# Optimization experiments

Measured on AMD Instinct MI355X. Metric: run time of the kernel, lower is better.

The kernel has to match this reference:

```python
import jax, jax.numpy as jnp
import numpy as np

B = 16; V = 30522; D = 512; H = 8; DH = 64; FF = 2048
NC = 4; NF = 30; NN = 34; FL = 64; HL = 32; NLAYERS = 2

def _pos_encoding(L, d):
    pos = np.arange(L)[:, None].astype(np.float32)
    i = np.arange(0, d, 2)[None, :].astype(np.float32)
    ang = pos / np.power(10000.0, i / d)
    pe = np.zeros((L, d), dtype=np.float32)
    pe[:, 0::2] = np.sin(ang)
    pe[:, 1::2] = np.cos(ang)
    return jnp.asarray(pe)

def _ln(x, g, b):
    m = x.mean(-1, keepdims=True)
    v = ((x - m) ** 2).mean(-1, keepdims=True)
    return (x - m) / jnp.sqrt(v + 1e-5) * g + b

def _encoder(ids, emb, Wqkv, bqkv, Wo, bo, ln1_g, ln1_b, Wff1, bff1, Wff2, bff2, ln2_g, ln2_b):
    Bx, L = ids.shape
    x = emb[ids] * jnp.sqrt(jnp.float32(D)) + _pos_encoding(L, D)
    for l in range(NLAYERS):  # torch post-norm encoder layer, relu FFN
        qkv = x @ Wqkv[l] + bqkv[l]
        q, k, v = jnp.split(qkv, 3, axis=-1)
        q = q.reshape(Bx, L, H, DH); k = k.reshape(Bx, L, H, DH); v = v.reshape(Bx, L, H, DH)
        att = jax.nn.softmax(jnp.einsum('blhd,bmhd->bhlm', q, k) / jnp.sqrt(jnp.float32(DH)), axis=-1)
        o = jnp.einsum('bhlm,bmhd->blhd', att, v).reshape(Bx, L, D) @ Wo[l] + bo[l]
        x = _ln(x + o, ln1_g[l], ln1_b[l])
        f = jax.nn.relu(x @ Wff1[l] + bff1[l]) @ Wff2[l] + bff2[l]
        x = _ln(x + f, ln2_g[l], ln2_b[l])
    return x

def _masked_mean(emb, mask):
    m = mask[..., None]
    return (emb * m).sum(1) / jnp.clip(m.sum(1), 1e-9, None)

def _solve_edges(W, adj, iters=100, lr=0.05, c=10.0):
    # differentiable proxy for the CvxpyLayer SDP relaxation: projected gradient
    # ascent on symmetric E in [0,1], maximizing sum(W*E) with quadratic penalties
    # for sum(adj*E) <= 6 and trace(E[:4,:4]) == 1 (PSD constraint dropped).
    diag4 = jnp.zeros((NN, NN)).at[jnp.arange(NC), jnp.arange(NC)].set(1.0)
    E0 = jnp.full(W.shape, 0.5)
    def step(E, _):
        s = jnp.sum(adj * E, axis=(1, 2), keepdims=True)
        d = jnp.sum(E * diag4, axis=(1, 2), keepdims=True)
        g = W - 2.0 * c * jax.nn.relu(s - 6.0) * adj - 2.0 * c * (d - 1.0) * diag4
        En = E + lr * g
        En = jnp.clip(0.5 * (En + jnp.swapaxes(En, 1, 2)), 0.0, 1.0)
        return En, None
    E, _ = jax.lax.scan(step, E0, None, length=iters)
    return E

def setup_inputs():
    key = jax.random.key(0)
    ks = jax.random.split(key, 24)
    w = lambda k, shape: (jax.random.normal(k, shape) * 0.02).astype(jnp.float32)
    return {
        'hypothesis_input_ids': jax.random.randint(ks[0], (B, NC, HL), 0, V),
        'hypothesis_attention_mask': jnp.ones((B, NC, HL), jnp.float32),
        'fact_attention_mask': jnp.ones((B, NF, FL), jnp.float32),
        'fact_input_ids': jax.random.randint(ks[1], (B, NF, FL), 0, V),
        'grounding_grounding_overlap': jax.random.uniform(ks[2], (B, NN, NN)),
        'abstract_abstract_overlap': jax.random.uniform(ks[3], (B, NN, NN)),
        'abstract_abstract_similarity': jax.random.uniform(ks[4], (B, NN, NN)),
        'question_grounding_overlap': jax.random.uniform(ks[5], (B, NN, NN)),
        'question_abstract_overlap': jax.random.uniform(ks[6], (B, NN, NN)),
        'question_abstract_similarity': jax.random.uniform(ks[7], (B, NN, NN)),
        'grounding_abstract_overlap': jax.random.uniform(ks[8], (B, NN, NN)),
        'question_question_score': w(ks[9], (B, NN, NN)),
        'labels': jax.random.randint(ks[10], (B,), 0, NC),
        'gold_similarity_scores': jax.random.normal(ks[11], (B, NC, NF)),
        'emb_table': w(ks[12], (V, D)),
        'Wqkv': w(ks[13], (NLAYERS, D, 3 * D)), 'bqkv': jnp.zeros((NLAYERS, 3 * D)),
        'Wo': w(ks[14], (NLAYERS, D, D)), 'bo': jnp.zeros((NLAYERS, D)),
        'ln1_g': jnp.ones((NLAYERS, D)), 'ln1_b': jnp.zeros((NLAYERS, D)),
        'Wff1': w(ks[15], (NLAYERS, D, FF)), 'bff1': jnp.zeros((NLAYERS, FF)),
        'Wff2': w(ks[16], (NLAYERS, FF, D)), 'bff2': jnp.zeros((NLAYERS, D)),
        'ln2_g': jnp.ones((NLAYERS, D)), 'ln2_b': jnp.zeros((NLAYERS, D)),
        'score_W': w(ks[17], (4 * D,)), 'score_b': jnp.zeros(()),
        'abs_score_W': w(ks[18], (4 * D,)), 'abs_score_b': jnp.zeros(()),
        'p_aa_overlap': jnp.ones(()), 'p_aa_sim': jnp.ones(()),
        'p_qa_overlap': jnp.ones(()), 'p_qa_sim': jnp.ones(()),
    }

def reference(hypothesis_input_ids, hypothesis_attention_mask, fact_attention_mask, fact_input_ids,
              grounding_grounding_overlap, abstract_abstract_overlap, abstract_abstract_similarity,
              question_grounding_overlap, question_abstract_overlap, question_abstract_similarity,
              grounding_abstract_overlap, question_question_score, labels, gold_similarity_scores,
              emb_table, Wqkv, bqkv, Wo, bo, ln1_g, ln1_b, Wff1, bff1, Wff2, bff2, ln2_g, ln2_b,
              score_W, score_b, abs_score_W, abs_score_b, p_aa_overlap, p_aa_sim, p_qa_overlap, p_qa_sim):
    enc = lambda ids: _encoder(ids, emb_table, Wqkv, bqkv, Wo, bo, ln1_g, ln1_b,
                               Wff1, bff1, Wff2, bff2, ln2_g, ln2_b)
    fseq = _masked_mean(enc(fact_input_ids.reshape(-1, FL)),
                        fact_attention_mask.reshape(-1, FL)).reshape(-1, NF, D)
    hseq = _masked_mean(enc(hypothesis_input_ids.reshape(-1, HL)),
                        hypothesis_attention_mask.reshape(-1, HL)).reshape(-1, NC, D)
    # abstract-abstract pairwise: concat(f_j, f_i, |f_j-f_i|, f_j*f_i) @ abs_score_W, done chunk-wise
    A1, A2, A3, A4 = jnp.split(abs_score_W, 4)
    aa = (fseq @ A1)[:, None, :] + (fseq @ A2)[:, :, None] \
       + jnp.einsum('bijd,d->bij', jnp.abs(fseq[:, None, :, :] - fseq[:, :, None, :]), A3) \
       + jnp.einsum('bid,bjd->bij', fseq * A4, fseq) + abs_score_b
    aa_sm = jax.nn.softmax(aa.reshape(-1, NF * NF), axis=1).reshape(-1, NF, NF)
    aa_sm = aa_sm * (1.0 - jnp.eye(NF))  # zero diagonal
    aa_sim = abstract_abstract_similarity.at[:, NC:, NC:].set(aa_sm)
    # question-abstract pairwise: concat(f_k, h_c, |f_k-h_c|, f_k*h_c) @ score_W
    S1, S2, S3, S4 = jnp.split(score_W, 4)
    qa = (fseq @ S1)[:, None, :] + (hseq @ S2)[:, :, None] \
       + jnp.einsum('bckd,d->bck', jnp.abs(fseq[:, None, :, :] - hseq[:, :, None, :]), S3) \
       + jnp.einsum('bkd,bcd->bck', fseq * S4, hseq) + score_b
    similarity_scores = jax.nn.softmax(qa, axis=2)  # [B, NC, NF]
    qa_sim = jnp.zeros_like(grounding_abstract_overlap)
    qa_sim = qa_sim.at[:, NC:, :NC].set(jnp.transpose(similarity_scores, (0, 2, 1)))
    qa_sim = qa_sim.at[:, :NC, NC:].set(similarity_scores)
    edge_weights = (-p_aa_overlap * abstract_abstract_overlap + p_aa_sim * aa_sim
                    + p_qa_overlap * question_abstract_overlap + p_qa_sim * qa_sim
                    + question_question_score)
    adj = (edge_weights != 0).astype(jnp.float32)
    edges = _solve_edges(edge_weights, adj)
    final_pred = jnp.diagonal(edges[:, :NC, :NC], axis1=1, axis2=2)  # [B, NC]
    gold = jax.nn.softmax(gold_similarity_scores, axis=2)
    logp = jax.nn.log_softmax(final_pred, axis=1)
    ce = -jnp.mean(logp[jnp.arange(final_pred.shape[0]), labels])
    mse = jnp.mean((similarity_scores - gold) ** 2)
    return ce + mse, final_pred
```

## Files before the change

### kernel.cpp

```cpp
#include <hip/hip_runtime.h>
#include <cstdint>
#include <cstddef>


using u16 = unsigned short;

typedef __bf16 bf16x8 __attribute__((ext_vector_type(8)));
typedef float  floatx4 __attribute__((ext_vector_type(4)));

#if defined(__has_builtin)
#if __has_builtin(__builtin_amdgcn_global_load_lds)
#define USE_GLL 1
#endif
#endif

__device__ __forceinline__ float bf2f(u16 u) {
  return __uint_as_float(((unsigned)u) << 16);
}
__device__ __forceinline__ u16 f2bf(float f) {
  unsigned u = __float_as_uint(f);
  u += 0x7FFFu + ((u >> 16) & 1u);
  return (u16)(u >> 16);
}
__device__ __forceinline__ float ldf(const void* p, size_t i, int isb) {
  return isb ? bf2f(((const u16*)p)[i]) : ((const float*)p)[i];
}

__device__ __forceinline__ float waveSum(float v) {
#pragma unroll
  for (int o = 32; o > 0; o >>= 1) v += __shfl_xor(v, o, 64);
  return v;
}
__device__ __forceinline__ float waveMax(float v) {
#pragma unroll
  for (int o = 32; o > 0; o >>= 1) v = fmaxf(v, __shfl_xor(v, o, 64));
  return v;
}
__device__ __forceinline__ float blockSum(float v, float* sh4) {
  v = waveSum(v);
  if ((threadIdx.x & 63) == 0) sh4[threadIdx.x >> 6] = v;
  __syncthreads();
  float r = sh4[0] + sh4[1] + sh4[2] + sh4[3];
  __syncthreads();
  return r;
}
__device__ __forceinline__ float blockMax(float v, float* sh4) {
  v = waveMax(v);
  if ((threadIdx.x & 63) == 0) sh4[threadIdx.x >> 6] = v;
  __syncthreads();
  float r = fmaxf(fmaxf(sh4[0], sh4[1]), fmaxf(sh4[2], sh4[3]));
  __syncthreads();
  return r;
}

__global__ void detect_kernel(const void* __restrict__ ln1g, int* __restrict__ flag) {
  unsigned u = *(const unsigned*)ln1g;
  *flag = (u == 0x3F800000u) ? 0 : 1;
}

__global__ __launch_bounds__(256) void pe_kernel(float* __restrict__ petab) {
  const int pos = blockIdx.x;
  const float LOG1E4_OVER_D = 9.210340371976184f / 512.0f;
  for (int d = threadIdx.x; d < 512; d += 256) {
    int i2 = d & ~1;
    float ang = (float)pos * expf(-(float)i2 * LOG1E4_OVER_D);
    petab[pos * 512 + d] = (d & 1) ? cosf(ang) : sinf(ang);
  }
}

__global__ __launch_bounds__(256) void transpose_kernel(const void* __restrict__ src,
                                                        u16* __restrict__ dst,
                                                        int K, int N,
                                                        size_t srcz, size_t dstz,
                                                        const int* __restrict__ F) {
  const int isb = *F;
  __shared__ u16 tile[32][33];
  size_t eoff = (size_t)blockIdx.z * srcz;
  u16* d = dst + (size_t)blockIdx.z * dstz;
  int bx = blockIdx.x, by = blockIdx.y;
  int tx = threadIdx.x & 31, ty = threadIdx.x >> 5;
  for (int i = ty; i < 32; i += 8)
    tile[i][tx] = f2bf(ldf(src, eoff + (size_t)(by * 32 + i) * N + bx * 32 + tx, isb));
  __syncthreads();
  for (int i = ty; i < 32; i += 8)
    d[(size_t)(bx * 32 + i) * K + by * 32 + tx] = tile[tx][i];
}

__global__ __launch_bounds__(256) void embed_kernel(const int* __restrict__ ids,
                                                    const void* __restrict__ emb,
                                                    u16* __restrict__ x, int L,
                                                    const float* __restrict__ petab,
                                                    const int* __restrict__ F) {
  const int isb = *F;
  int tok = blockIdx.x;
  int pos = tok % L;
  int id = ids[tok];
  for (int d = threadIdx.x; d < 512; d += 256) {
    float e = ldf(emb, (size_t)id * 512 + d, isb) * 22.62741699796952f;
    x[(size_t)tok * 512 + d] = f2bf(e + petab[pos * 512 + d]);
  }
}

__global__ __launch_bounds__(256) void embed2_kernel(const int* __restrict__ fids,
                                                     const int* __restrict__ hids,
                                                     const void* __restrict__ emb,
                                                     u16* __restrict__ x,
                                                     const float* __restrict__ petab,
                                                     const int* __restrict__ F) {
  const int isb = *F;
  int tok = blockIdx.x;
  int id, pos;
  if (tok < 30720) { id = fids[tok]; pos = tok & 63; }
  else             { int t2 = tok - 30720; id = hids[t2]; pos = t2 & 31; }
  for (int d = threadIdx.x; d < 512; d += 256) {
    float e = ldf(emb, (size_t)id * 512 + d, isb) * 22.62741699796952f;
    x[(size_t)tok * 512 + d] = f2bf(e + petab[pos * 512 + d]);
  }
}

template <int RELU>
__global__ __launch_bounds__(256, 2) void gemm_bt(const u16* __restrict__ A,
                                                  const u16* __restrict__ Bt,
                                                  const void* __restrict__ bias,
                                                  u16* __restrict__ C,
                                                  int M, int N, int K, size_t boff,
                                                  const int* __restrict__ F) {
  const int isb = *F;
  __shared__ __align__(16) u16 As[128 * 64];
  __shared__ __align__(16) u16 Bs[128 * 64];
  const int tid = threadIdx.x;
  const int lane = tid & 63;
  const int wave = tid >> 6;
  const int wm = wave >> 1, wn = wave & 1;
  const int l15 = lane & 15, quad = lane >> 4;

  const int nwg = gridDim.x * gridDim.y;
  const int hw  = blockIdx.y * gridDim.x + blockIdx.x;
  int lg;
  if ((nwg & 7) == 0) {
    lg = (hw & 7) * (nwg >> 3) + (hw >> 3);
  } else {
    int q = nwg >> 3, r = nwg & 7;
    int xcd = hw & 7, j = hw >> 3;
    lg = (xcd < r ? xcd * (q + 1) : r * (q + 1) + (xcd - r) * q) + j;
  }
  const int bm = lg / gridDim.x;
  const int bn = lg - bm * gridDim.x;

  floatx4 acc[4][4];
#pragma unroll
  for (int i = 0; i < 4; i++)
#pragma unroll
    for (int j = 0; j < 4; j++) acc[i][j] = (floatx4){0.f, 0.f, 0.f, 0.f};

  const u16* Abase = A + (size_t)bm * 128 * K;
  const u16* Bbase = Bt + (size_t)bn * 128 * K;

  for (int kt = 0; kt < K; kt += 64) {
#pragma unroll
    for (int i = 0; i < 4; i++) {
      int c = i * 256 + tid;
      int row = c >> 3, p = c & 7;
      int col = (((p - row) & 7)) * 8;
      const u16* ga = &Abase[(size_t)row * K + kt + col];
      const u16* gb = &Bbase[(size_t)row * K + kt + col];
#ifdef USE_GLL
      __builtin_amdgcn_global_load_lds(
          (const __attribute__((address_space(1))) void*)ga,
          (__attribute__((address_space(3))) void*)&As[c * 8], 16, 0, 0);
      __builtin_amdgcn_global_load_lds(
          (const __attribute__((address_space(1))) void*)gb,
          (__attribute__((address_space(3))) void*)&Bs[c * 8], 16, 0, 0);
#else
      *(uint4*)&As[c * 8] = *(const uint4*)ga;
      *(uint4*)&Bs[c * 8] = *(const uint4*)gb;
#endif
    }
    __syncthreads();
#pragma unroll
    for (int ks = 0; ks < 2; ks++) {
      bf16x8 af[4], bfr[4];
#pragma unroll
      for (int mi = 0; mi < 4; mi++) {
        int ra = wm * 64 + mi * 16 + l15;
        int q = ks * 4 + quad;
        af[mi] = *(const bf16x8*)&As[ra * 64 + ((q + ra) & 7) * 8];
      }
#pragma unroll
      for (int ni = 0; ni < 4; ni++) {
        int rb = wn * 64 + ni * 16 + l15;
        int q = ks * 4 + quad;
        bfr[ni] = *(const bf16x8*)&Bs[rb * 64 + ((q + rb) & 7) * 8];
      }
#pragma unroll
      for (int mi = 0; mi < 4; mi++)
#pragma unroll
        for (int ni = 0; ni < 4; ni++)
          acc[mi][ni] = __builtin_amdgcn_mfma_f32_16x16x32_bf16(af[mi], bfr[ni], acc[mi][ni], 0, 0, 0);
    }
    __syncthreads();
  }

  float bv[4];
  const int gcb = bn * 128 + wn * 64 + l15;
#pragma unroll
  for (int ni = 0; ni < 4; ni++) bv[ni] = ldf(bias, boff + gcb + ni * 16, isb);
#pragma unroll
  for (int mi = 0; mi < 4; mi++) {
#pragma unroll
    for (int r = 0; r < 4; r++) {
      int grow = bm * 128 + wm * 64 + mi * 16 + quad * 4 + r;
      size_t rb = (size_t)grow * N + gcb;
#pragma unroll
      for (int ni = 0; ni < 4; ni++) {
        float v = acc[mi][ni][r] + bv[ni];
        if (RELU) v = fmaxf(v, 0.f);
        C[rb + ni * 16] = f2bf(v);
      }
    }
  }
}

__global__ __launch_bounds__(256) void attn_kernel(const u16* __restrict__ qkv,
                                                   u16* __restrict__ o, int L,
                                                   int nblk1,
                                                   const u16* __restrict__ qkv2,
                                                   u16* __restrict__ o2, int L2) {
  int bid = blockIdx.x;
  if (bid >= nblk1) { qkv = qkv2; o = o2; L = L2; bid -= nblk1; }
  const int h = bid & 7;
  const int s = bid >> 3;
  __shared__ __align__(16) u16 Qs[64 * 72];
  __shared__ __align__(16) u16 Ks[64 * 72];
  __shared__ __align__(16) u16 Vt[64 * 72];
  __shared__ float Ss[64 * 66];
  const int tid = threadIdx.x;
  const int lane = tid & 63;
  const int wave = tid >> 6;
  const int wm = wave >> 1, wn = wave & 1;
  const int l15 = lane & 15, quad = lane >> 4;
  const int base = s * L;

  for (int idx = tid; idx < 512; idx += 256) {
    int t = idx >> 3, d8 = (idx & 7) * 8;
    if (t < L) {
      size_t g = (size_t)(base + t) * 1536 + h * 64 + d8;
      *(uint4*)&Qs[t * 72 + d8] = *(const uint4*)&qkv[g];
      *(uint4*)&Ks[t * 72 + d8] = *(const uint4*)&qkv[g + 512];
      u16 vv[8];
      *(uint4*)vv = *(const uint4*)&qkv[g + 1024];
#pragma unroll
      for (int i = 0; i < 8; i++) Vt[(d8 + i) * 72 + t] = vv[i];
    } else {
      uint4 z = {0u, 0u, 0u, 0u};
      *(uint4*)&Qs[t * 72 + d8] = z;
      *(uint4*)&Ks[t * 72 + d8] = z;
#pragma unroll
      for (int i = 0; i < 8; i++) Vt[(d8 + i) * 72 + t] = 0;
    }
  }
  __syncthreads();

  {
    floatx4 acc[2][2];
#pragma unroll
    for (int mi = 0; mi < 2; mi++)
#pragma unroll
      for (int ni = 0; ni < 2; ni++) acc[mi][ni] = (floatx4){0.f, 0.f, 0.f, 0.f};
#pragma unroll
    for (int ks = 0; ks < 2; ks++) {
      bf16x8 af[2], bfr[2];
#pragma unroll
      for (int mi = 0; mi < 2; mi++)
        af[mi] = *(const bf16x8*)&Qs[(wm * 32 + mi * 16 + l15) * 72 + ks * 32 + quad * 8];
#pragma unroll
      for (int ni = 0; ni < 2; ni++)
        bfr[ni] = *(const bf16x8*)&Ks[(wn * 32 + ni * 16 + l15) * 72 + ks * 32 + quad * 8];
#pragma unroll
      for (int mi = 0; mi < 2; mi++)
#pragma unroll
        for (int ni = 0; ni < 2; ni++)
          acc[mi][ni] = __builtin_amdgcn_mfma_f32_16x16x32_bf16(af[mi], bfr[ni], acc[mi][ni], 0, 0, 0);
    }
#pragma unroll
    for (int mi = 0; mi < 2; mi++)
#pragma unroll
      for (int ni = 0; ni < 2; ni++)
#pragma unroll
        for (int r = 0; r < 4; r++)
          Ss[(wm * 32 + mi * 16 + quad * 4 + r) * 66 + wn * 32 + ni * 16 + l15] =
              acc[mi][ni][r] * 0.125f;
  }
  __syncthreads();

  {
    int r = tid >> 2, sub = tid & 3;
    int j0 = sub * 16;
    float mx = -3.4e38f;
    if (r < L)
      for (int j = j0; j < j0 + 16; j++)
        if (j < L) mx = fmaxf(mx, Ss[r * 66 + j]);
    mx = fmaxf(mx, __shfl_xor(mx, 1, 64));
    mx = fmaxf(mx, __shfl_xor(mx, 2, 64));
    float sum = 0.f;
    if (r < L)
      for (int j = j0; j < j0 + 16; j++)
        if (j < L) { float e = expf(Ss[r * 66 + j] - mx); Ss[r * 66 + j] = e; sum += e; }
    sum += __shfl_xor(sum, 1, 64);
    sum += __shfl_xor(sum, 2, 64);
    float inv = 1.f / sum;
    if (r < L)
      for (int j = j0; j < j0 + 16; j++)
        Qs[r * 72 + j] = (j < L) ? f2bf(Ss[r * 66 + j] * inv) : (u16)0;
  }
  __syncthreads();

  {
    floatx4 acc[2][2];
#pragma unroll
    for (int mi = 0; mi < 2; mi++)
#pragma unroll
      for (int ni = 0; ni < 2; ni++) acc[mi][ni] = (floatx4){0.f, 0.f, 0.f, 0.f};
#pragma unroll
    for (int ks = 0; ks < 2; ks++) {
      bf16x8 af[2], bfr[2];
#pragma unroll
      for (int mi = 0; mi < 2; mi++)
        af[mi] = *(const bf16x8*)&Qs[(wm * 32 + mi * 16 + l15) * 72 + ks * 32 + quad * 8];
#pragma unroll
      for (int ni = 0; ni < 2; ni++)
        bfr[ni] = *(const bf16x8*)&Vt[(wn * 32 + ni * 16 + l15) * 72 + ks * 32 + quad * 8];
#pragma unroll
      for (int mi = 0; mi < 2; mi++)
#pragma unroll
        for (int ni = 0; ni < 2; ni++)
          acc[mi][ni] = __builtin_amdgcn_mfma_f32_16x16x32_bf16(af[mi], bfr[ni], acc[mi][ni], 0, 0, 0);
    }
#pragma unroll
    for (int mi = 0; mi < 2; mi++) {
#pragma unroll
      for (int r = 0; r < 4; r++) {
        int t = wm * 32 + mi * 16 + quad * 4 + r;
        if (t < L) {
#pragma unroll
          for (int ni = 0; ni < 2; ni++) {
            int d = wn * 32 + ni * 16 + l15;
            o[(size_t)(base + t) * 512 + h * 64 + d] = f2bf(acc[mi][ni][r]);
          }
        }
      }
    }
  }
}

__global__ __launch_bounds__(256) void add_ln_kernel(u16* __restrict__ x,
                                                     const u16* __restrict__ y,
                                                     const void* __restrict__ g,
                                                     const void* __restrict__ b,
                                                     size_t eoff,
                                                     const int* __restrict__ F) {
  const int isb = *F;
  const int row = blockIdx.x, tid = threadIdx.x;
  __shared__ float sh[4];
  size_t o0 = (size_t)row * 512 + tid * 2;
  unsigned xv = *(const unsigned*)&x[o0];
  unsigned yv = *(const unsigned*)&y[o0];
  float v0 = bf2f((u16)xv) + bf2f((u16)yv);
  float v1 = bf2f((u16)(xv >> 16)) + bf2f((u16)(yv >> 16));
  float mean = blockSum(v0 + v1, sh) * (1.f / 512.f);
  float d0 = v0 - mean, d1 = v1 - mean;
  float var = blockSum(d0 * d0 + d1 * d1, sh) * (1.f / 512.f);
  float rstd = rsqrtf(var + 1e-5f);
  float g0 = ldf(g, eoff + tid * 2, isb),     g1 = ldf(g, eoff + tid * 2 + 1, isb);
  float b0 = ldf(b, eoff + tid * 2, isb),     b1 = ldf(b, eoff + tid * 2 + 1, isb);
  unsigned r0 = f2bf(d0 * rstd * g0 + b0);
  unsigned r1 = f2bf(d1 * rstd * g1 + b1);
  *(unsigned*)&x[o0] = r0 | (r1 << 16);
}

__global__ __launch_bounds__(256) void pool_kernel(const u16* __restrict__ x,
                                                   const void* __restrict__ mask,
                                                   float* __restrict__ pooled, int L,
                                                   size_t moff,
                                                   const int* __restrict__ F) {
  const int isb = *F;
  const int s = blockIdx.x;
  float msum = 0.f;
  for (int t = 0; t < L; t++) msum += ldf(mask, moff + s * L + t, isb);
  float inv = 1.f / fmaxf(msum, 1e-9f);
  for (int d = threadIdx.x; d < 512; d += 256) {
    float acc = 0.f;
    for (int t = 0; t < L; t++)
      acc += bf2f(x[(size_t)(s * L + t) * 512 + d]) * ldf(mask, moff + s * L + t, isb);
    pooled[(size_t)s * 512 + d] = acc * inv;
  }
}

__global__ __launch_bounds__(256) void pool2_kernel(const u16* __restrict__ xf,
                                                    const void* __restrict__ fmask,
                                                    float* __restrict__ fpool,
                                                    const u16* __restrict__ xh,
                                                    const void* __restrict__ hmask,
                                                    float* __restrict__ hpool,
                                                    const int* __restrict__ F) {
  const int isb = *F;
  const u16* x; const void* mask; float* pooled; int L, s;
  if (blockIdx.x < 480) { x = xf; mask = fmask; pooled = fpool; L = 64; s = blockIdx.x; }
  else                  { x = xh; mask = hmask; pooled = hpool; L = 32; s = blockIdx.x - 480; }
  float msum = 0.f;
  for (int t = 0; t < L; t++) msum += ldf(mask, (size_t)s * L + t, isb);
  float inv = 1.f / fmaxf(msum, 1e-9f);
  for (int d = threadIdx.x; d < 512; d += 256) {
    float acc = 0.f;
    for (int t = 0; t < L; t++)
      acc += bf2f(x[(size_t)(s * L + t) * 512 + d]) * ldf(mask, (size_t)s * L + t, isb);
    pooled[(size_t)s * 512 + d] = acc * inv;
  }
}

__global__ __launch_bounds__(64) void pair_score_kernel(const float* __restrict__ X,
                                                        const float* __restrict__ Y,
                                                        const void* __restrict__ Wv,
                                                        const void* __restrict__ bscal,
                                                        float* __restrict__ outp,
                                                        int NI, int NJ,
                                                        const int* __restrict__ F) {
  const int isb = *F;
  int gid = blockIdx.x;
  int j = gid % NJ;
  int t = gid / NJ;
  int i = t % NI;
  int b = t / NI;
  const float* xv = X + ((size_t)b * NI + i) * 512;
  const float* yv = Y + ((size_t)b * NJ + j) * 512;
  int l = threadIdx.x;
  float p = 0.f;
  for (int d = l; d < 512; d += 64) {
    float xi = xv[d], yj = yv[d];
    p += ldf(Wv, d, isb) * yj + ldf(Wv, 512 + d, isb) * xi +
         ldf(Wv, 1024 + d, isb) * fabsf(yj - xi) + ldf(Wv, 1536 + d, isb) * xi * yj;
  }
  p = waveSum(p);
  if (l == 0) outp[gid] = p + ldf(bscal, 0, isb);
}

__global__ __launch_bounds__(256) void aa_softmax_kernel(const float* __restrict__ aa,
                                                         float* __restrict__ aasm) {
  const int b = blockIdx.x;
  const float* src = aa + (size_t)b * 900;
  float* dst = aasm + (size_t)b * 900;
  __shared__ float sh[4];
  int tid = threadIdx.x;
  float mx = -3.4e38f;
  for (int i = tid; i < 900; i += 256) mx = fmaxf(mx, src[i]);
  mx = blockMax(mx, sh);
  float sum = 0.f;
  for (int i = tid; i < 900; i += 256) sum += expf(src[i] - mx);
  sum = blockSum(sum, sh);
  float inv = 1.f / sum;
  for (int i = tid; i < 900; i += 256) {
    int r = i / 30, c = i - r * 30;
    dst[i] = (r == c) ? 0.f : expf(src[i] - mx) * inv;
  }
}

__global__ __launch_bounds__(64) void qa_softmax_kernel(const float* __restrict__ qa,
                                                        float* __restrict__ sim) {
  int g = blockIdx.x;
  int l = threadIdx.x;
  float v = (l < 30) ? qa[(size_t)g * 30 + l] : -3.4e38f;
  float mx = waveMax(v);
  float e = (l < 30) ? expf(v - mx) : 0.f;
  float s = waveSum(e);
  if (l < 30) sim[(size_t)g * 30 + l] = e / s;
}

__global__ __launch_bounds__(256) void edgew_kernel(const void* __restrict__ aaov,
                                                    const void* __restrict__ aasim_in,
                                                    const void* __restrict__ qaov,
                                                    const void* __restrict__ qq,
                                                    const float* __restrict__ aasm,
                                                    const float* __restrict__ sim,
                                                    const void* __restrict__ p1,
                                                    const void* __restrict__ p2,
                                                    const void* __restrict__ p3,
                                                    const void* __restrict__ p4,
                                                    float* __restrict__ Wout,
                                                    const int* __restrict__ F) {
  const int isb = *F;
  int e = blockIdx.x * 256 + threadIdx.x;
  if (e >= 16 * 1156) return;
  int b = e / 1156;
  int rem = e - b * 1156;
  int r = rem / 34, c = rem - r * 34;
  float aas;
  if (r >= 4 && c >= 4) aas = aasm[(size_t)b * 900 + (r - 4) * 30 + (c - 4)];
  else                  aas = ldf(aasim_in, e, isb);
  float qas = 0.f;
  if (r >= 4 && c < 4)      qas = sim[((size_t)b * 4 + c) * 30 + (r - 4)];
  else if (r < 4 && c >= 4) qas = sim[((size_t)b * 4 + r) * 30 + (c - 4)];
  float w = -ldf(p1, 0, isb) * ldf(aaov, e, isb) + ldf(p2, 0, isb) * aas +
            ldf(p3, 0, isb) * ldf(qaov, e, isb) + ldf(p4, 0, isb) * qas +
            ldf(qq, e, isb);
  Wout[e] = w;
}

__global__ __launch_bounds__(64) void solve_kernel(const float* __restrict__ Wmat,
                                                   float* __restrict__ pred,
                                                   float* __restrict__ outp) {
  const int b = blockIdx.x;
  const int lane = threadIdx.x;
  float E[19], Ws[19], As[19];
  bool dg[19];
#pragma unroll
  for (int k = 0; k < 19; k++) {
    int e = lane + (k << 6);
    if (e < 1156) {
      int r = e / 34, c = e - r * 34;
      float w1 = Wmat[(size_t)b * 1156 + e];
      float w2 = Wmat[(size_t)b * 1156 + c * 34 + r];
      Ws[k] = 0.5f * (w1 + w2);
      As[k] = 0.5f * (((w1 != 0.f) ? 1.f : 0.f) + ((w2 != 0.f) ? 1.f : 0.f));
      dg[k] = (r == c && r < 4);
      E[k] = 0.5f;
    } else {
      Ws[k] = 0.f; As[k] = 0.f; dg[k] = false; E[k] = 0.f;
    }
  }
  for (int it = 0; it < 100; it++) {
    float ps = 0.f;
#pragma unroll
    for (int k = 0; k < 19; k++) ps += As[k] * E[k];
    float s = waveSum(ps);
    float dd = __shfl(E[0], 0, 64) + __shfl(E[0], 35, 64) +
               __shfl(E[1], 6, 64) + __shfl(E[1], 41, 64);
    float coef_s = (s > 6.f) ? 20.f * (s - 6.f) : 0.f;
    float coef_d = 20.f * (dd - 1.f);
#pragma unroll
    for (int k = 0; k < 19; k++) {
      float g = Ws[k] - coef_s * As[k] - (dg[k] ? coef_d : 0.f);
      E[k] = fminf(fmaxf(E[k] + 0.05f * g, 0.f), 1.f);
    }
  }
  float v0 = E[0], v1 = E[1];
  if (lane == 0)  { pred[b * 4 + 0] = v0; outp[1 + b * 4 + 0] = v0; }
  if (lane == 35) { pred[b * 4 + 1] = v0; outp[1 + b * 4 + 1] = v0; }
  if (lane == 6)  { pred[b * 4 + 2] = v1; outp[1 + b * 4 + 2] = v1; }
  if (lane == 41) { pred[b * 4 + 3] = v1; outp[1 + b * 4 + 3] = v1; }
}

__global__ __launch_bounds__(256) void loss_kernel(const float* __restrict__ sim,
                                                   const void* __restrict__ gold,
                                                   const float* __restrict__ pred,
                                                   const int* __restrict__ labels,
                                                   float* __restrict__ outp,
                                                   const int* __restrict__ F) {
  const int isb = *F;
  __shared__ float sh[4];
  const int tid = threadIdx.x;
  float local = 0.f;
  if (tid < 64) {
    float mx = -3.4e38f;
    for (int k = 0; k < 30; k++) mx = fmaxf(mx, ldf(gold, (size_t)tid * 30 + k, isb));
    float sum = 0.f;
    for (int k = 0; k < 30; k++) sum += expf(ldf(gold, (size_t)tid * 30 + k, isb) - mx);
    float inv = 1.f / sum;
    for (int k = 0; k < 30; k++) {
      float gsm = expf(ldf(gold, (size_t)tid * 30 + k, isb) - mx) * inv;
      float d = sim[(size_t)tid * 30 + k] - gsm;
      local += d * d;
    }
  }
  float mse = blockSum(local, sh) * (1.f / 1920.f);
  float cel = 0.f;
  if (tid < 16) {
    const float* f = pred + tid * 4;
    int lb = labels[tid] & 3;
    float mx = fmaxf(fmaxf(f[0], f[1]), fmaxf(f[2], f[3]));
    float lse = logf(expf(f[0] - mx) + expf(f[1] - mx) + expf(f[2] - mx) + expf(f[3] - mx));
    float lp = f[lb] - mx - lse;
    cel = -lp * (1.f / 16.f);
  }
  float ce = blockSum(cel, sh);
  if (tid == 0) outp[0] = ce + mse;
}

extern "C" void kernel_launch(void* const* d_in, const int* in_sizes, int n_in,
                              void* d_out, int out_size, void* d_ws, size_t ws_size,
                              hipStream_t stream) {
  (void)in_sizes; (void)n_in; (void)out_size;
  const int*  hyp_ids   = (const int*)d_in[0];
  const void* hyp_mask  = d_in[1];
  const void* fact_mask = d_in[2];
  const int*  fact_ids  = (const int*)d_in[3];
  const void* aa_ov     = d_in[5];
  const void* aa_sim_in = d_in[6];
  const void* qa_ov     = d_in[8];
  const void* qq        = d_in[11];
  const int*  labels    = (const int*)d_in[12];
  const void* gold      = d_in[13];
  const void* emb       = d_in[14];
  const void* Wqkv      = d_in[15];
  const void* bqkv      = d_in[16];
  const void* Wo        = d_in[17];
  const void* bo        = d_in[18];
  const void* ln1g      = d_in[19];
  const void* ln1b      = d_in[20];
  const void* Wff1      = d_in[21];
  const void* bff1      = d_in[22];
  const void* Wff2      = d_in[23];
  const void* bff2      = d_in[24];
  const void* ln2g      = d_in[25];
  const void* ln2b      = d_in[26];
  const void* scoreW    = d_in[27];
  const void* scoreB    = d_in[28];
  const void* absW      = d_in[29];
  const void* absB      = d_in[30];
  const void* p_aaov    = d_in[31];
  const void* p_aasim   = d_in[32];
  const void* p_qaov    = d_in[33];
  const void* p_qasim   = d_in[34];
  float* out = (float*)d_out;

  char* ws = (char*)d_ws;
  size_t off = 0;
  auto alloc = [&](size_t bytes) -> void* {
    void* p = ws + off;
    off += (bytes + 255) & ~(size_t)255;
    return p;
  };

  float* PRED = (float*)alloc(64ull * 4);
  int*   FLAG = (int*)alloc(256);
  float* SIM  = (float*)alloc(16ull * 120 * 4);
  float* QA   = (float*)alloc(16ull * 120 * 4);
  float* AASM = (float*)alloc(16ull * 900 * 4);
  float* AA   = (float*)alloc(16ull * 900 * 4);
  float* WMAT = (float*)alloc(16ull * 1156 * 4);
  float* FSEQ = (float*)alloc(480ull * 512 * 4);
  float* HSEQ = (float*)alloc(64ull * 512 * 4);
  float* PETAB= (float*)alloc(64ull * 512 * 4);
  u16* WT_QKV = (u16*)alloc(2ull * 1536 * 512 * 2);
  u16* WT_O   = (u16*)alloc(2ull * 512 * 512 * 2);
  u16* WT_F1  = (u16*)alloc(2ull * 2048 * 512 * 2);
  u16* WT_F2  = (u16*)alloc(2ull * 512 * 2048 * 2);

  const int opts_tok[6] = {32768, 30720, 15360, 10240, 6144, 3072};
  const int opts_nch[6] = {1, 1, 2, 3, 5, 10};
  int CH_TOK = 3072, NCH = 10;
  for (int i = 0; i < 6; i++) {
    size_t need = off + (size_t)opts_tok[i] * 7168 + 4096;
    if (need <= ws_size) { CH_TOK = opts_tok[i]; NCH = opts_nch[i]; break; }
  }
  u16* X   = (u16*)alloc((size_t)CH_TOK * 512 * 2);
  u16* BIG = (u16*)alloc((size_t)CH_TOK * 2048 * 2);
  u16* ATT = (u16*)alloc((size_t)CH_TOK * 512 * 2);
  u16* Y   = (u16*)alloc((size_t)CH_TOK * 512 * 2);

  detect_kernel<<<1, 1, 0, stream>>>(ln1g, FLAG);
  pe_kernel<<<64, 256, 0, stream>>>(PETAB);

  transpose_kernel<<<dim3(48, 16, 2), 256, 0, stream>>>(
      Wqkv, WT_QKV, 512, 1536, 512ull * 1536, 1536ull * 512, FLAG);
  transpose_kernel<<<dim3(16, 16, 2), 256, 0, stream>>>(
      Wo, WT_O, 512, 512, 512ull * 512, 512ull * 512, FLAG);
  transpose_kernel<<<dim3(64, 16, 2), 256, 0, stream>>>(
      Wff1, WT_F1, 512, 2048, 512ull * 2048, 2048ull * 512, FLAG);
  transpose_kernel<<<dim3(16, 64, 2), 256, 0, stream>>>(
      Wff2, WT_F2, 2048, 512, 2048ull * 512, 512ull * 2048, FLAG);

  if (CH_TOK >= 32768) {
    const int M = 32768;
    const size_t HOFF = 30720;
    embed2_kernel<<<M, 256, 0, stream>>>(fact_ids, hyp_ids, emb, X, PETAB, FLAG);
    for (int l = 0; l < 2; l++) {
      gemm_bt<0><<<dim3(12, M / 128), 256, 0, stream>>>(
          X, WT_QKV + (size_t)l * 1536 * 512, bqkv, BIG, M, 1536, 512,
          (size_t)l * 1536, FLAG);
      attn_kernel<<<480 * 8 + 64 * 8, 256, 0, stream>>>(
          BIG, ATT, 64, 480 * 8, BIG + HOFF * 1536, ATT + HOFF * 512, 32);
      gemm_bt<0><<<dim3(4, M / 128), 256, 0, stream>>>(
          ATT, WT_O + (size_t)l * 512 * 512, bo, Y, M, 512, 512,
          (size_t)l * 512, FLAG);
      add_ln_kernel<<<M, 256, 0, stream>>>(X, Y, ln1g, ln1b, (size_t)l * 512, FLAG);
      gemm_bt<1><<<dim3(16, M / 128), 256, 0, stream>>>(
          X, WT_F1 + (size_t)l * 2048 * 512, bff1, BIG, M, 2048, 512,
          (size_t)l * 2048, FLAG);
      gemm_bt<0><<<dim3(4, M / 128), 256, 0, stream>>>(
          BIG, WT_F2 + (size_t)l * 512 * 2048, bff2, Y, M, 512, 2048,
          (size_t)l * 512, FLAG);
      add_ln_kernel<<<M, 256, 0, stream>>>(X, Y, ln2g, ln2b, (size_t)l * 512, FLAG);
    }
    pool2_kernel<<<544, 256, 0, stream>>>(X, fact_mask, FSEQ,
                                          X + HOFF * 512, hyp_mask, HSEQ, FLAG);
  } else {
    auto encode = [&](const int* ids, int nseq, int L, const void* mask,
                      size_t moff, float* pooled) {
      int M = nseq * L;
      embed_kernel<<<M, 256, 0, stream>>>(ids, emb, X, L, PETAB, FLAG);
      for (int l = 0; l < 2; l++) {
        gemm_bt<0><<<dim3(12, M / 128), 256, 0, stream>>>(
            X, WT_QKV + (size_t)l * 1536 * 512, bqkv, BIG, M, 1536, 512,
            (size_t)l * 1536, FLAG);
        attn_kernel<<<nseq * 8, 256, 0, stream>>>(BIG, ATT, L, nseq * 8, BIG, ATT, L);
        gemm_bt<0><<<dim3(4, M / 128), 256, 0, stream>>>(
            ATT, WT_O + (size_t)l * 512 * 512, bo, Y, M, 512, 512,
            (size_t)l * 512, FLAG);
        add_ln_kernel<<<M, 256, 0, stream>>>(X, Y, ln1g, ln1b, (size_t)l * 512, FLAG);
        gemm_bt<1><<<dim3(16, M / 128), 256, 0, stream>>>(
            X, WT_F1 + (size_t)l * 2048 * 512, bff1, BIG, M, 2048, 512,
            (size_t)l * 2048, FLAG);
        gemm_bt<0><<<dim3(4, M / 128), 256, 0, stream>>>(
            BIG, WT_F2 + (size_t)l * 512 * 2048, bff2, Y, M, 512, 2048,
            (size_t)l * 512, FLAG);
        add_ln_kernel<<<M, 256, 0, stream>>>(X, Y, ln2g, ln2b, (size_t)l * 512, FLAG);
      }
      pool_kernel<<<nseq, 256, 0, stream>>>(X, mask, pooled, L, moff, FLAG);
    };
    const int seq_per = 480 / NCH;
    for (int c = 0; c < NCH; c++) {
      encode(fact_ids + (size_t)c * seq_per * 64, seq_per, 64, fact_mask,
             (size_t)c * seq_per * 64, FSEQ + (size_t)c * seq_per * 512);
    }
    encode(hyp_ids, 64, 32, hyp_mask, 0, HSEQ);
  }

  pair_score_kernel<<<16 * 30 * 30, 64, 0, stream>>>(FSEQ, FSEQ, absW, absB, AA, 30, 30, FLAG);
  pair_score_kernel<<<16 * 4 * 30, 64, 0, stream>>>(HSEQ, FSEQ, scoreW, scoreB, QA, 4, 30, FLAG);
  aa_softmax_kernel<<<16, 256, 0, stream>>>(AA, AASM);
  qa_softmax_kernel<<<64, 64, 0, stream>>>(QA, SIM);

  edgew_kernel<<<(16 * 1156 + 255) / 256, 256, 0, stream>>>(
      aa_ov, aa_sim_in, qa_ov, qq, AASM, SIM, p_aaov, p_aasim, p_qaov, p_qasim,
      WMAT, FLAG);
  solve_kernel<<<16, 64, 0, stream>>>(WMAT, PRED, out);
  loss_kernel<<<1, 256, 0, stream>>>(SIM, gold, PRED, labels, out, FLAG);
}
```

Baseline: 990.2 us.

## Vectorize embed and layernorm to wave-per-row, swizzle V transpose, merge small kernels

```diff
diff --git a/kernel.cpp b/kernel.cpp
--- a/kernel.cpp
+++ b/kernel.cpp
@@ -24,6 +24,20 @@
 }
 __device__ __forceinline__ float ldf(const void* p, size_t i, int isb) {
   return isb ? bf2f(((const u16*)p)[i]) : ((const float*)p)[i];
+}
+__device__ __forceinline__ void unpack8(uint4 v, float* f) {
+  f[0] = bf2f((u16)v.x); f[1] = bf2f((u16)(v.x >> 16));
+  f[2] = bf2f((u16)v.y); f[3] = bf2f((u16)(v.y >> 16));
+  f[4] = bf2f((u16)v.z); f[5] = bf2f((u16)(v.z >> 16));
+  f[6] = bf2f((u16)v.w); f[7] = bf2f((u16)(v.w >> 16));
+}
+__device__ __forceinline__ uint4 pack8(const float* f) {
+  uint4 v;
+  v.x = (unsigned)f2bf(f[0]) | ((unsigned)f2bf(f[1]) << 16);
+  v.y = (unsigned)f2bf(f[2]) | ((unsigned)f2bf(f[3]) << 16);
+  v.z = (unsigned)f2bf(f[4]) | ((unsigned)f2bf(f[5]) << 16);
+  v.w = (unsigned)f2bf(f[6]) | ((unsigned)f2bf(f[7]) << 16);
+  return v;
 }
 
 __device__ __forceinline__ float waveSum(float v) {
@@ -108,14 +122,26 @@
                                                      const float* __restrict__ petab,
                                                      const int* __restrict__ F) {
   const int isb = *F;
-  int tok = blockIdx.x;
+  const int lane = threadIdx.x & 63;
+  const size_t tok = (size_t)blockIdx.x * 4 + (threadIdx.x >> 6);
   int id, pos;
-  if (tok < 30720) { id = fids[tok]; pos = tok & 63; }
-  else             { int t2 = tok - 30720; id = hids[t2]; pos = t2 & 31; }
-  for (int d = threadIdx.x; d < 512; d += 256) {
-    float e = ldf(emb, (size_t)id * 512 + d, isb) * 22.62741699796952f;
-    x[(size_t)tok * 512 + d] = f2bf(e + petab[pos * 512 + d]);
-  }
+  if (tok < 30720) { id = fids[tok]; pos = (int)(tok & 63); }
+  else             { size_t t2 = tok - 30720; id = hids[t2]; pos = (int)(t2 & 31); }
+  const int d0 = lane * 8;
+  float e[8];
+  if (isb) {
+    unpack8(*(const uint4*)((const u16*)emb + (size_t)id * 512 + d0), e);
+  } else {
+    const float* ep = (const float*)emb + (size_t)id * 512 + d0;
+    float4 a = *(const float4*)ep, c = *(const float4*)(ep + 4);
+    e[0] = a.x; e[1] = a.y; e[2] = a.z; e[3] = a.w;
+    e[4] = c.x; e[5] = c.y; e[6] = c.z; e[7] = c.w;
+  }
+  const float* pe = petab + (size_t)pos * 512 + d0;
+  float o[8];
+#pragma unroll
+  for (int k = 0; k < 8; k++) o[k] = e[k] * 22.62741699796952f + pe[k];
+  *(uint4*)&x[tok * 512 + d0] = pack8(o);
 }
 
 template <int RELU>
@@ -243,6 +269,7 @@
 
   for (int idx = tid; idx < 512; idx += 256) {
     int t = idx >> 3, d8 = (idx & 7) * 8;
+    int rot = ((t >> 3) + (idx & 7)) & 7;
     if (t < L) {
       size_t g = (size_t)(base + t) * 1536 + h * 64 + d8;
       *(uint4*)&Qs[t * 72 + d8] = *(const uint4*)&qkv[g];
@@ -250,13 +277,13 @@
       u16 vv[8];
       *(uint4*)vv = *(const uint4*)&qkv[g + 1024];
 #pragma unroll
-      for (int i = 0; i < 8; i++) Vt[(d8 + i) * 72 + t] = vv[i];
+      for (int i = 0; i < 8; i++) Vt[(d8 + i) * 72 + rot * 8 + (t & 7)] = vv[i];
     } else {
       uint4 z = {0u, 0u, 0u, 0u};
       *(uint4*)&Qs[t * 72 + d8] = z;
       *(uint4*)&Ks[t * 72 + d8] = z;
 #pragma unroll
-      for (int i = 0; i < 8; i++) Vt[(d8 + i) * 72 + t] = 0;
+      for (int i = 0; i < 8; i++) Vt[(d8 + i) * 72 + rot * 8 + (t & 7)] = 0;
     }
   }
   __syncthreads();
@@ -328,8 +355,11 @@
       for (int mi = 0; mi < 2; mi++)
         af[mi] = *(const bf16x8*)&Qs[(wm * 32 + mi * 16 + l15) * 72 + ks * 32 + quad * 8];
 #pragma unroll
-      for (int ni = 0; ni < 2; ni++)
-        bfr[ni] = *(const bf16x8*)&Vt[(wn * 32 + ni * 16 + l15) * 72 + ks * 32 + quad * 8];
+      for (int ni = 0; ni < 2; ni++) {
+        int rb = wn * 32 + ni * 16 + l15;
+        int p = ((ks * 4 + quad) + (rb >> 3)) & 7;
+        bfr[ni] = *(const bf16x8*)&Vt[rb * 72 + p * 8];
+      }
 #pragma unroll
       for (int mi = 0; mi < 2; mi++)
 #pragma unroll
@@ -360,22 +390,26 @@
                                                      size_t eoff,
                                                      const int* __restrict__ F) {
   const int isb = *F;
-  const int row = blockIdx.x, tid = threadIdx.x;
-  __shared__ float sh[4];
-  size_t o0 = (size_t)row * 512 + tid * 2;
-  unsigned xv = *(const unsigned*)&x[o0];
-  unsigned yv = *(const unsigned*)&y[o0];
-  float v0 = bf2f((u16)xv) + bf2f((u16)yv);
-  float v1 = bf2f((u16)(xv >> 16)) + bf2f((u16)(yv >> 16));
-  float mean = blockSum(v0 + v1, sh) * (1.f / 512.f);
-  float d0 = v0 - mean, d1 = v1 - mean;
-  float var = blockSum(d0 * d0 + d1 * d1, sh) * (1.f / 512.f);
-  float rstd = rsqrtf(var + 1e-5f);
-  float g0 = ldf(g, eoff + tid * 2, isb),     g1 = ldf(g, eoff + tid * 2 + 1, isb);
-  float b0 = ldf(b, eoff + tid * 2, isb),     b1 = ldf(b, eoff + tid * 2 + 1, isb);
-  unsigned r0 = f2bf(d0 * rstd * g0 + b0);
-  unsigned r1 = f2bf(d1 * rstd * g1 + b1);
-  *(unsigned*)&x[o0] = r0 | (r1 << 16);
+  const int lane = threadIdx.x & 63;
+  const size_t row = (size_t)blockIdx.x * 4 + (threadIdx.x >> 6);
+  const int d0 = lane * 8;
+  size_t o0 = row * 512 + d0;
+  float xv[8], yv[8], v[8];
+  unpack8(*(const uint4*)&x[o0], xv);
+  unpack8(*(const uint4*)&y[o0], yv);
+  float s = 0.f;
+#pragma unroll
+  for (int k = 0; k < 8; k++) { v[k] = xv[k] + yv[k]; s += v[k]; }
+  float mean = waveSum(s) * (1.f / 512.f);
+  float q = 0.f;
+#pragma unroll
+  for (int k = 0; k < 8; k++) { v[k] -= mean; q += v[k] * v[k]; }
+  float rstd = rsqrtf(waveSum(q) * (1.f / 512.f) + 1e-5f);
+  float o[8];
+#pragma unroll
+  for (int k = 0; k < 8; k++)
+    o[k] = v[k] * rstd * ldf(g, eoff + d0 + k, isb) + ldf(b, eoff + d0 + k, isb);
+  *(uint4*)&x[o0] = pack8(o);
 }
 
 __global__ __launch_bounds__(256) void pool_kernel(const u16* __restrict__ x,
@@ -418,15 +452,20 @@
   }
 }
 
-__global__ __launch_bounds__(64) void pair_score_kernel(const float* __restrict__ X,
-                                                        const float* __restrict__ Y,
-                                                        const void* __restrict__ Wv,
-                                                        const void* __restrict__ bscal,
-                                                        float* __restrict__ outp,
-                                                        int NI, int NJ,
-                                                        const int* __restrict__ F) {
+__global__ __launch_bounds__(64) void pair2_kernel(const float* __restrict__ FS,
+                                                   const float* __restrict__ HS,
+                                                   const void* __restrict__ absW,
+                                                   const void* __restrict__ absB,
+                                                   const void* __restrict__ scW,
+                                                   const void* __restrict__ scB,
+                                                   float* __restrict__ AA,
+                                                   float* __restrict__ QA,
+                                                   const int* __restrict__ F) {
   const int isb = *F;
   int gid = blockIdx.x;
+  const float *X, *Y; const void *Wv, *bs; float* outp; int NI, NJ;
+  if (gid < 14400) { X = FS; Y = FS; Wv = absW; bs = absB; outp = AA; NI = 30; NJ = 30; }
+  else { gid -= 14400; X = HS; Y = FS; Wv = scW; bs = scB; outp = QA; NI = 4; NJ = 30; }
   int j = gid % NJ;
   int t = gid / NJ;
   int i = t % NI;
@@ -441,38 +480,39 @@
          ldf(Wv, 1024 + d, isb) * fabsf(yj - xi) + ldf(Wv, 1536 + d, isb) * xi * yj;
   }
   p = waveSum(p);
-  if (l == 0) outp[gid] = p + ldf(bscal, 0, isb);
-}
-
-__global__ __launch_bounds__(256) void aa_softmax_kernel(const float* __restrict__ aa,
-                                                         float* __restrict__ aasm) {
-  const int b = blockIdx.x;
-  const float* src = aa + (size_t)b * 900;
-  float* dst = aasm + (size_t)b * 900;
+  if (l == 0) outp[gid] = p + ldf(bs, 0, isb);
+}
+
+__global__ __launch_bounds__(256) void sm2_kernel(const float* __restrict__ aa,
+                                                  float* __restrict__ aasm,
+                                                  const float* __restrict__ qa,
+                                                  float* __restrict__ sim) {
   __shared__ float sh[4];
-  int tid = threadIdx.x;
-  float mx = -3.4e38f;
-  for (int i = tid; i < 900; i += 256) mx = fmaxf(mx, src[i]);
-  mx = blockMax(mx, sh);
-  float sum = 0.f;
-  for (int i = tid; i < 900; i += 256) sum += expf(src[i] - mx);
-  sum = blockSum(sum, sh);
-  float inv = 1.f / sum;
-  for (int i = tid; i < 900; i += 256) {
-    int r = i / 30, c = i - r * 30;
-    dst[i] = (r == c) ? 0.f : expf(src[i] - mx) * inv;
-  }
-}
-
-__global__ __launch_bounds__(64) void qa_softmax_kernel(const float* __restrict__ qa,
-                                                        float* __restrict__ sim) {
-  int g = blockIdx.x;
-  int l = threadIdx.x;
-  float v = (l < 30) ? qa[(size_t)g * 30 + l] : -3.4e38f;
-  float mx = waveMax(v);
-  float e = (l < 30) ? expf(v - mx) : 0.f;
-  float s = waveSum(e);
-  if (l < 30) sim[(size_t)g * 30 + l] = e / s;
+  if (blockIdx.x < 16) {
+    const int b = blockIdx.x;
+    const float* src = aa + (size_t)b * 900;
+    float* dst = aasm + (size_t)b * 900;
+    int tid = threadIdx.x;
+    float mx = -3.4e38f;
+    for (int i = tid; i < 900; i += 256) mx = fmaxf(mx, src[i]);
+    mx = blockMax(mx, sh);
+    float sum = 0.f;
+    for (int i = tid; i < 900; i += 256) sum += expf(src[i] - mx);
+    sum = blockSum(sum, sh);
+    float inv = 1.f / sum;
+    for (int i = tid; i < 900; i += 256) {
+      int r = i / 30, c = i - r * 30;
+      dst[i] = (r == c) ? 0.f : expf(src[i] - mx) * inv;
+    }
+  } else {
+    int g = (blockIdx.x - 16) * 4 + (threadIdx.x >> 6);
+    int l = threadIdx.x & 63;
+    float v = (l < 30) ? qa[(size_t)g * 30 + l] : -3.4e38f;
+    float mx = waveMax(v);
+    float e = (l < 30) ? expf(v - mx) : 0.f;
+    float s = waveSum(e);
+    if (l < 30) sim[(size_t)g * 30 + l] = e / s;
+  }
 }
 
 __global__ __launch_bounds__(256) void edgew_kernel(const void* __restrict__ aaov,
@@ -672,7 +712,7 @@
   if (CH_TOK >= 32768) {
     const int M = 32768;
     const size_t HOFF = 30720;
-    embed2_kernel<<<M, 256, 0, stream>>>(fact_ids, hyp_ids, emb, X, PETAB, FLAG);
+    embed2_kernel<<<M / 4, 256, 0, stream>>>(fact_ids, hyp_ids, emb, X, PETAB, FLAG);
     for (int l = 0; l < 2; l++) {
       gemm_bt<0><<<dim3(12, M / 128), 256, 0, stream>>>(
           X, WT_QKV + (size_t)l * 1536 * 512, bqkv, BIG, M, 1536, 512,
@@ -682,14 +722,14 @@
       gemm_bt<0><<<dim3(4, M / 128), 256, 0, stream>>>(
           ATT, WT_O + (size_t)l * 512 * 512, bo, Y, M, 512, 512,
           (size_t)l * 512, FLAG);
-      add_ln_kernel<<<M, 256, 0, stream>>>(X, Y, ln1g, ln1b, (size_t)l * 512, FLAG);
+      add_ln_kernel<<<M / 4, 256, 0, stream>>>(X, Y, ln1g, ln1b, (size_t)l * 512, FLAG);
       gemm_bt<1><<<dim3(16, M / 128), 256, 0, stream>>>(
           X, WT_F1 + (size_t)l * 2048 * 512, bff1, BIG, M, 2048, 512,
           (size_t)l * 2048, FLAG);
       gemm_bt<0><<<dim3(4, M / 128), 256, 0, stream>>>(
           BIG, WT_F2 + (size_t)l * 512 * 2048, bff2, Y, M, 512, 2048,
           (size_t)l * 512, FLAG);
-      add_ln_kernel<<<M, 256, 0, stream>>>(X, Y, ln2g, ln2b, (size_t)l * 512, FLAG);
+      add_ln_kernel<<<M / 4, 256, 0, stream>>>(X, Y, ln2g, ln2b, (size_t)l * 512, FLAG);
     }
     pool2_kernel<<<544, 256, 0, stream>>>(X, fact_mask, FSEQ,
                                           X + HOFF * 512, hyp_mask, HSEQ, FLAG);
@@ -706,14 +746,14 @@
         gemm_bt<0><<<dim3(4, M / 128), 256, 0, stream>>>(
             ATT, WT_O + (size_t)l * 512 * 512, bo, Y, M, 512, 512,
             (size_t)l * 512, FLAG);
-        add_ln_kernel<<<M, 256, 0, stream>>>(X, Y, ln1g, ln1b, (size_t)l * 512, FLAG);
+        add_ln_kernel<<<M / 4, 256, 0, stream>>>(X, Y, ln1g, ln1b, (size_t)l * 512, FLAG);
         gemm_bt<1><<<dim3(16, M / 128), 256, 0, stream>>>(
             X, WT_F1 + (size_t)l * 2048 * 512, bff1, BIG, M, 2048, 512,
             (size_t)l * 2048, FLAG);
         gemm_bt<0><<<dim3(4, M / 128), 256, 0, stream>>>(
             BIG, WT_F2 + (size_t)l * 512 * 2048, bff2, Y, M, 512, 2048,
             (size_t)l * 512, FLAG);
-        add_ln_kernel<<<M, 256, 0, stream>>>(X, Y, ln2g, ln2b, (size_t)l * 512, FLAG);
+        add_ln_kernel<<<M / 4, 256, 0, stream>>>(X, Y, ln2g, ln2b, (size_t)l * 512, FLAG);
       }
       pool_kernel<<<nseq, 256, 0, stream>>>(X, mask, pooled, L, moff, FLAG);
     };
@@ -725,10 +765,9 @@
     encode(hyp_ids, 64, 32, hyp_mask, 0, HSEQ);
   }
 
-  pair_score_kernel<<<16 * 30 * 30, 64, 0, stream>>>(FSEQ, FSEQ, absW, absB, AA, 30, 30, FLAG);
-  pair_score_kernel<<<16 * 4 * 30, 64, 0, stream>>>(HSEQ, FSEQ, scoreW, scoreB, QA, 4, 30, FLAG);
-  aa_softmax_kernel<<<16, 256, 0, stream>>>(AA, AASM);
-  qa_softmax_kernel<<<64, 64, 0, stream>>>(QA, SIM);
+  pair2_kernel<<<16 * 30 * 30 + 16 * 4 * 30, 64, 0, stream>>>(
+      FSEQ, HSEQ, absW, absB, scoreW, scoreB, AA, QA, FLAG);
+  sm2_kernel<<<32, 256, 0, stream>>>(AA, AASM, QA, SIM);
 
   edgew_kernel<<<(16 * 1156 + 255) / 256, 256, 0, stream>>>(
       aa_ov, aa_sim_in, qa_ov, qq, AASM, SIM, p_aaov, p_aasim, p_qaov, p_qasim,
```

After: 1.080 ms. 1.09x slower.
